# Kernel tuning notes

Hardware: AMD Instinct MI355X
Metric: run time of the kernel (lower is better)

## Reference

```python
import jax, jax.numpy as jnp
import numpy as np

K = 5
PAD = K // 2
EPS = 1e-12  # F.normalize eps


def setup_inputs() -> dict:
    key = jax.random.key(0)
    k1, k2, k3 = jax.random.split(key, 3)
    b, c, h, w = 8, 1024, 64, 64
    out_ch = 1024
    feature = jax.random.normal(k1, (b, c, h, w), dtype=jnp.float32)
    # Conv2d(1024 + K*K, out_ch, 1) -> weight [out_ch, 1049], bias [out_ch]
    conv_w = jax.random.normal(k2, (out_ch, c + K * K), dtype=jnp.float32) * 0.02
    conv_b = jax.random.normal(k3, (out_ch,), dtype=jnp.float32) * 0.02
    return {"feature": feature, "conv_w": conv_w, "conv_b": conv_b}


def reference(feature, conv_w, conv_b):
    b, c, h, w = feature.shape
    # L2-normalize over channel dim (F.normalize: x / max(||x||, eps))
    norm = jnp.sqrt(jnp.sum(feature * feature, axis=1, keepdims=True))
    fn = feature / jnp.maximum(norm, EPS)
    fp = jnp.pad(fn, ((0, 0), (0, 0), (PAD, PAD), (PAD, PAD)))
    # 25 shifted correlations; order matches torch loop: index = col*K + row
    corr = jnp.stack(
        [jnp.sum(fp[:, :, r:h + r, cc:w + cc] * fn, axis=1)
         for cc in range(K) for r in range(K)],
        axis=1,
    )  # [b, K*K, h, w]
    cat = jnp.concatenate([feature, corr], axis=1)  # [b, c+K*K, h, w]
    y = jnp.einsum('oc,bchw->bohw', conv_w, cat) + conv_b[None, :, None, None]
    return jax.nn.relu(y)
```

## Files before the change

### kernel.cpp

```cpp
#include <hip/hip_runtime.h>
#include <hip/hip_bf16.h>


typedef __attribute__((ext_vector_type(8))) short short8x;
typedef __attribute__((ext_vector_type(4))) float floatx4;

#define B_   8
#define C_   1024
#define HW_  4096
#define KPAD 1088
#define NT   17

__device__ __forceinline__ unsigned short f2bf(float f) {
  unsigned int u = __float_as_uint(f);
  u += 0x7FFFu + ((u >> 16) & 1u);
  return (unsigned short)(u >> 16);
}

__device__ __forceinline__ void async16(const void* g, void* l) {
  __builtin_amdgcn_global_load_lds(
      (__attribute__((address_space(1))) void*)(void*)g,
      (__attribute__((address_space(3))) void*)l, 16, 0, 0);
}

__device__ __forceinline__ short8x rd16(const char* p) {
  return *(const short8x*)p;
}

__global__ __launch_bounds__(512) void scn_aux(
    const float* __restrict__ f, float* __restrict__ part,
    unsigned short* __restrict__ At) {
  __shared__ float lds2[2][64][65];
  const int n = blockIdx.x;
  const int g = n / 9, r = n - g * 9;
  const int tid = threadIdx.x;

  if (r == 0) {
    const int x = tid & 63;
    const int y = (g & 7) * 8 + (tid >> 6);
    const int cs = (g >> 3) & 7, b = g >> 6;

    const int xs0 = (x + 2 < 64) ? x + 2 : 63;
    const int xs1 = (x + 1 < 64) ? x + 1 : 63;
    const int xs3 = (x - 1 >= 0) ? x - 1 : 0;
    const int xs4 = (x - 2 >= 0) ? x - 2 : 0;

    const bool ym2 = (y >= 2), ym1 = (y >= 1), yp1 = (y <= 62), yp2 = (y <= 61);

    const float* rp0 = f + ((size_t)b * C_ + cs * 128) * HW_ + y * 64;

    float h[25];
#pragma unroll
    for (int j = 0; j < 25; ++j) h[j] = 0.f;

#pragma unroll 4
    for (int c = 0; c < 128; ++c) {
      const float* rp = rp0 + (size_t)c * HW_;
      const float ctr = rp[x];
      const float vm2 = ym2 ? rp[x - 128] : 0.f;
      const float vm1 = ym1 ? rp[x - 64] : 0.f;
      const float vp1 = yp1 ? rp[x + 64] : 0.f;
      const float vp2 = yp2 ? rp[x + 128] : 0.f;
      const float c0 = __shfl(ctr, xs0, 64);
      const float c1 = __shfl(ctr, xs1, 64);
      const float c3 = __shfl(ctr, xs3, 64);
      const float c4 = __shfl(ctr, xs4, 64);
      const float v[5] = {vm2, vm1, ctr, vp1, vp2};
      const float cc[5] = {c0, c1, ctr, c3, c4};
#pragma unroll
      for (int dxi = 0; dxi < 5; ++dxi)
#pragma unroll
        for (int dyi = 0; dyi < 5; ++dyi)
          h[dxi * 5 + dyi] = fmaf(v[dyi], cc[dxi], h[dxi * 5 + dyi]);
    }

    float* pb = part + (size_t)(cs * 25) * 32768 + b * HW_ + y * 64;
#pragma unroll
    for (int j = 0; j < 25; ++j) {
      const int dx = (j / 5) - 2;
      const int tgt = x - dx;
      const int wx = (tgt + 64) & 63;
      const float val = ((unsigned)tgt < 64u) ? h[j] : 0.f;
      pb[(size_t)j * 32768 + wx] = val;
    }
  } else {
    const int half = tid >> 8, t256 = tid & 255;
    const int tile = (g * 8 + (r - 1)) * 2 + half;
    const int b = tile >> 10, rem = tile & 1023;
    const int kt = rem >> 6, mt = rem & 63;

    const float* src = f + ((size_t)b * C_ + kt * 64) * HW_ + mt * 64;
    const int mi = t256 & 63, kr = t256 >> 6;
#pragma unroll
    for (int i = 0; i < 16; ++i)
      lds2[half][kr + i * 4][mi] = src[(size_t)(kr + i * 4) * HW_ + mi];
    __syncthreads();
    unsigned short* dst = At + ((size_t)b * HW_ + mt * 64) * KPAD + kt * 64;
    const int c = t256 & 7, mr = t256 >> 3;
#pragma unroll
    for (int h2 = 0; h2 < 2; ++h2) {
      const int mm = mr + h2 * 32;
      short8x v;
#pragma unroll
      for (int j = 0; j < 8; ++j) v[j] = (short)f2bf(lds2[half][c * 8 + j][mm]);
      *(short8x*)(dst + (size_t)mm * KPAD + c * 8) = v;
    }
  }
}

__global__ __launch_bounds__(256) void scn_invn(const float* __restrict__ part,
                                                float* __restrict__ invn) {
  const int i = blockIdx.x * 256 + threadIdx.x;
  float s = 0.f;
#pragma unroll
  for (int cs = 0; cs < 8; ++cs) s += part[(size_t)(cs * 25 + 12) * 32768 + i];
  invn[i] = 1.0f / fmaxf(sqrtf(s), 1e-12f);
}

__global__ __launch_bounds__(256) void scn_corr_reduce(
    const float* __restrict__ part, const float* __restrict__ invn,
    unsigned short* __restrict__ At) {
  const int b = blockIdx.y;
  const int m = blockIdx.x * 256 + threadIdx.x;
  const int i = b * HW_ + m;
  const int y = m >> 6, x = m & 63;

  float acc[25];
#pragma unroll
  for (int j = 0; j < 25; ++j) acc[j] = 0.f;
#pragma unroll 1
  for (int cs = 0; cs < 8; ++cs) {
    const float* pb = part + (size_t)(cs * 25) * 32768 + i;
#pragma unroll
    for (int j = 0; j < 25; ++j) acc[j] += pb[(size_t)j * 32768];
  }
  const float ic = invn[i];
  unsigned short r[64];
#pragma unroll
  for (int j = 0; j < 25; ++j) {
    const int dy = (j % 5) - 2, dx = (j / 5) - 2;
    const int ny = y + dy, nx = x + dx;
    float in2 = (ny >= 0 && ny < 64 && nx >= 0 && nx < 64)
                    ? invn[b * HW_ + (ny << 6) + nx] : 0.f;
    r[j] = f2bf(acc[j] * ic * in2);
  }
#pragma unroll
  for (int j = 25; j < 64; ++j) r[j] = 0;
  unsigned short* row = At + ((size_t)b * HW_ + m) * KPAD + 1024;
#pragma unroll
  for (int v = 0; v < 8; ++v) *(short8x*)(row + v * 8) = *(short8x*)(r + v * 8);
}

__global__ __launch_bounds__(256) void scn_wcast(const float* __restrict__ w,
                                                 unsigned short* __restrict__ Wb) {
  const int i = blockIdx.x * 256 + threadIdx.x;
  const int o = i / KPAD, k = i - o * KPAD;
  Wb[i] = (k < 1049) ? f2bf(w[(size_t)o * 1049 + k]) : 0;
}

__global__ __launch_bounds__(512, 2) void scn_gemm(
    const unsigned short* __restrict__ Wb, const unsigned short* __restrict__ At,
    const float* __restrict__ bias, float* __restrict__ out) {
  extern __shared__ char lds[];
  const int tid = threadIdx.x;
  const int l = tid & 63;
  const int wid = tid >> 6;
  const int wm = wid >> 2;
  const int wn = wid & 3;
  const int nb = blockIdx.x, ob = blockIdx.y, b = blockIdx.z;

  const int rr = tid >> 3;
  const int cswz = ((tid & 7) ^ (rr & 7)) << 3;
  const unsigned short* gA = Wb + (size_t)(ob * 256 + rr) * KPAD + cswz;
  const unsigned short* gB = At + ((size_t)b * HW_ + nb * 256 + rr) * KPAD + cswz;
  char* const dBase = (char*)lds + tid * 16;

#define ISSUE_A(bf, kt)                                         \
  do {                                                          \
    const unsigned short* _s = gA + (kt) * 64;                  \
    char* _d = dBase + (bf) * 65536;                            \
    async16(_s, _d);                                            \
    async16(_s + (size_t)64 * KPAD, _d + 8192);                 \
    async16(_s + (size_t)128 * KPAD, _d + 16384);               \
    async16(_s + (size_t)192 * KPAD, _d + 24576);               \
  } while (0)

#define ISSUE_B(bf, kt)                                         \
  do {                                                          \
    const unsigned short* _s = gB + (kt) * 64;                  \
    char* _d = dBase + (bf) * 65536 + 32768;                    \
    async16(_s, _d);                                            \
    async16(_s + (size_t)64 * KPAD, _d + 8192);                 \
    async16(_s + (size_t)128 * KPAD, _d + 16384);               \
    async16(_s + (size_t)192 * KPAD, _d + 24576);               \
  } while (0)

  const int l15 = l & 15, l4g = l >> 4, l7 = l & 7;
  const int aoff0 = l15 * 128 + ((l4g ^ l7) << 4);
  const int aoff1 = l15 * 128 + (((l4g + 4) ^ l7) << 4);
  const char* aB0 = (const char*)lds + wm * 16384;
  const char* bB0 = (const char*)lds + 32768 + (wn >> 1) * 16384 + (wn & 1) * 8192;

  floatx4 acc[8][4];
#pragma unroll
  for (int i = 0; i < 8; ++i)
#pragma unroll
    for (int j = 0; j < 4; ++j) acc[i][j] = (floatx4){0.f, 0.f, 0.f, 0.f};

  ISSUE_A(0, 0); ISSUE_B(0, 0);
  ISSUE_A(1, 1); ISSUE_B(1, 1);
  asm volatile("s_waitcnt vmcnt(8)" ::: "memory");
  __builtin_amdgcn_s_barrier();

  short8x a[4][2], b0[2][2], b1[2][2];

  for (int t = 0; t < NT; ++t) {
    const int bf = t & 1;
    const char* ab = aB0 + bf * 65536;
    const char* bb = bB0 + bf * 65536;
    const int t2 = (t < NT - 2) ? (t + 2) : 0;

#pragma unroll
    for (int i = 0; i < 4; ++i) {
      a[i][0] = rd16(ab + i * 2048 + aoff0);
      a[i][1] = rd16(ab + i * 2048 + aoff1);
    }
#pragma unroll
    for (int j = 0; j < 2; ++j) {
      b0[j][0] = rd16(bb + j * 2048 + aoff0);
      b0[j][1] = rd16(bb + j * 2048 + aoff1);
    }
    __builtin_amdgcn_s_barrier();
    asm volatile("s_waitcnt lgkmcnt(0)" ::: "memory");
    __builtin_amdgcn_sched_barrier(0);
    __builtin_amdgcn_s_setprio(1);
#pragma unroll
    for (int i = 0; i < 4; ++i)
#pragma unroll
      for (int j = 0; j < 2; ++j) {
        acc[i][j] = __builtin_amdgcn_mfma_f32_16x16x32_bf16(a[i][0], b0[j][0], acc[i][j], 0, 0, 0);
        acc[i][j] = __builtin_amdgcn_mfma_f32_16x16x32_bf16(a[i][1], b0[j][1], acc[i][j], 0, 0, 0);
      }
    __builtin_amdgcn_s_setprio(0);
    __builtin_amdgcn_s_barrier();

#pragma unroll
    for (int j = 0; j < 2; ++j) {
      b1[j][0] = rd16(bb + (2 + j) * 2048 + aoff0);
      b1[j][1] = rd16(bb + (2 + j) * 2048 + aoff1);
    }
    __builtin_amdgcn_s_barrier();
    asm volatile("s_waitcnt lgkmcnt(0)" ::: "memory");
    __builtin_amdgcn_sched_barrier(0);
    __builtin_amdgcn_s_setprio(1);
#pragma unroll
    for (int i = 0; i < 4; ++i)
#pragma unroll
      for (int j = 0; j < 2; ++j) {
        acc[i][2 + j] = __builtin_amdgcn_mfma_f32_16x16x32_bf16(a[i][0], b1[j][0], acc[i][2 + j], 0, 0, 0);
        acc[i][2 + j] = __builtin_amdgcn_mfma_f32_16x16x32_bf16(a[i][1], b1[j][1], acc[i][2 + j], 0, 0, 0);
      }
    __builtin_amdgcn_s_setprio(0);
    __builtin_amdgcn_s_barrier();

#pragma unroll
    for (int i = 0; i < 4; ++i) {
      a[i][0] = rd16(ab + (4 + i) * 2048 + aoff0);
      a[i][1] = rd16(ab + (4 + i) * 2048 + aoff1);
    }
    ISSUE_B(bf, t2);
    __builtin_amdgcn_s_barrier();
    asm volatile("s_waitcnt lgkmcnt(0)" ::: "memory");
    __builtin_amdgcn_sched_barrier(0);
    __builtin_amdgcn_s_setprio(1);
#pragma unroll
    for (int i = 0; i < 4; ++i)
#pragma unroll
      for (int j = 0; j < 2; ++j) {
        acc[4 + i][2 + j] = __builtin_amdgcn_mfma_f32_16x16x32_bf16(a[i][0], b1[j][0], acc[4 + i][2 + j], 0, 0, 0);
        acc[4 + i][2 + j] = __builtin_amdgcn_mfma_f32_16x16x32_bf16(a[i][1], b1[j][1], acc[4 + i][2 + j], 0, 0, 0);
      }
    __builtin_amdgcn_s_setprio(0);
    __builtin_amdgcn_s_barrier();

    ISSUE_A(bf, t2);
    __builtin_amdgcn_s_barrier();
    __builtin_amdgcn_s_setprio(1);
#pragma unroll
    for (int i = 0; i < 4; ++i)
#pragma unroll
      for (int j = 0; j < 2; ++j) {
        acc[4 + i][j] = __builtin_amdgcn_mfma_f32_16x16x32_bf16(a[i][0], b0[j][0], acc[4 + i][j], 0, 0, 0);
        acc[4 + i][j] = __builtin_amdgcn_mfma_f32_16x16x32_bf16(a[i][1], b0[j][1], acc[4 + i][j], 0, 0, 0);
      }
    __builtin_amdgcn_s_setprio(0);
    asm volatile("s_waitcnt vmcnt(8)" ::: "memory");
    __builtin_amdgcn_s_barrier();
  }
  asm volatile("s_waitcnt vmcnt(0)" ::: "memory");
#undef ISSUE_A
#undef ISSUE_B

  float* outb = out + (size_t)b * C_ * HW_;
#pragma unroll
  for (int i = 0; i < 8; ++i) {
    const int o0 = ob * 256 + wm * 128 + i * 16 + l4g * 4;
    float bs[4];
#pragma unroll
    for (int r = 0; r < 4; ++r) bs[r] = bias[o0 + r];
#pragma unroll
    for (int j = 0; j < 4; ++j) {
      const int m = nb * 256 + wn * 64 + j * 16 + l15;
#pragma unroll
      for (int r = 0; r < 4; ++r) {
        float v = acc[i][j][r] + bs[r];
        outb[(size_t)(o0 + r) * HW_ + m] = v > 0.f ? v : 0.f;
      }
    }
  }
}

extern "C" void kernel_launch(void* const* d_in, const int* in_sizes, int n_in,
                              void* d_out, int out_size, void* d_ws, size_t ws_size,
                              hipStream_t stream) {
  const float* feature = (const float*)d_in[0];
  const float* conv_w  = (const float*)d_in[1];
  const float* conv_b  = (const float*)d_in[2];
  float* out = (float*)d_out;

  char* ws = (char*)d_ws;
  unsigned short* At = (unsigned short*)(ws);
  float* part        = (float*)(ws + 71303168);
  unsigned short* Wb = (unsigned short*)(ws + 71303168);
  float* invn        = (float*)(ws + 97517568);

  static int gemm_attr_set = 0;
  if (!gemm_attr_set) {
    hipFuncSetAttribute((const void*)scn_gemm,
                        hipFuncAttributeMaxDynamicSharedMemorySize, 131072);
    gemm_attr_set = 1;
  }

  scn_aux<<<dim3(4608), 512, 0, stream>>>(feature, part, At);
  scn_invn<<<dim3(128), 256, 0, stream>>>(part, invn);
  scn_corr_reduce<<<dim3(16, 8), 256, 0, stream>>>(part, invn, At);
  scn_wcast<<<dim3((1024 * KPAD) / 256), 256, 0, stream>>>(conv_w, Wb);
  scn_gemm<<<dim3(16, 4, 8), 512, 131072, stream>>>(Wb, At, conv_b, out);
}
```

Baseline: 388.3 us.

## Fuse weight cast into aux kernel, atomically accumulate correlations, merge reduce kernels

Correlation partials from the eight channel slices are now summed with atomicAdd into one zeroed buffer instead of written as separate slices, so the separate inverse-norm pass is no longer needed. The inverse-norm and correlation-reduce kernels become one kernel that computes inverse norms for a row halo in LDS. The weight cast to bf16 moves into extra blocks of the aux kernel with 8-wide stores, and the transpose loads become float4. Together these cut kernel launches and traffic on the partial buffer, at the cost of a memset, atomic contention, and ordering nondeterminism in the float sums.

New measurement: 379.0 us. -2.4%, faster.

```diff
diff --git a/kernel.cpp b/kernel.cpp
--- a/kernel.cpp
+++ b/kernel.cpp
@@ -28,13 +28,27 @@
 }
 
 __global__ __launch_bounds__(512) void scn_aux(
-    const float* __restrict__ f, float* __restrict__ part,
-    unsigned short* __restrict__ At) {
+    const float* __restrict__ f, float* __restrict__ corr,
+    unsigned short* __restrict__ At, const float* __restrict__ w,
+    unsigned short* __restrict__ Wb) {
   __shared__ float lds2[2][64][65];
   const int n = blockIdx.x;
+  const int tid = threadIdx.x;
+
+  if (n >= 4608) {
+    const int base = (n - 4608) * 4096 + tid * 8;
+    const int o = base / KPAD, kk = base - o * KPAD;
+    short8x v;
+#pragma unroll
+    for (int e = 0; e < 8; ++e) {
+      const int k = kk + e;
+      v[e] = (k < 1049) ? (short)f2bf(w[(size_t)o * 1049 + k]) : (short)0;
+    }
+    *(short8x*)(Wb + (size_t)o * KPAD + kk) = v;
+    return;
+  }
+
   const int g = n / 9, r = n - g * 9;
-  const int tid = threadIdx.x;
-
   if (r == 0) {
     const int x = tid & 63;
     const int y = (g & 7) * 8 + (tid >> 6);
@@ -74,14 +88,14 @@
           h[dxi * 5 + dyi] = fmaf(v[dyi], cc[dxi], h[dxi * 5 + dyi]);
     }
 
-    float* pb = part + (size_t)(cs * 25) * 32768 + b * HW_ + y * 64;
+    float* pb = corr + b * HW_ + y * 64;
 #pragma unroll
     for (int j = 0; j < 25; ++j) {
       const int dx = (j / 5) - 2;
       const int tgt = x - dx;
       const int wx = (tgt + 64) & 63;
       const float val = ((unsigned)tgt < 64u) ? h[j] : 0.f;
-      pb[(size_t)j * 32768 + wx] = val;
+      atomicAdd(pb + (size_t)j * 32768 + wx, val);
     }
   } else {
     const int half = tid >> 8, t256 = tid & 255;
@@ -89,11 +103,14 @@
     const int b = tile >> 10, rem = tile & 1023;
     const int kt = rem >> 6, mt = rem & 63;
 
-    const float* src = f + ((size_t)b * C_ + kt * 64) * HW_ + mt * 64;
-    const int mi = t256 & 63, kr = t256 >> 6;
-#pragma unroll
-    for (int i = 0; i < 16; ++i)
-      lds2[half][kr + i * 4][mi] = src[(size_t)(kr + i * 4) * HW_ + mi];
+    const int m4 = (t256 & 15) << 2, kr0 = t256 >> 4;
+    const float* src = f + ((size_t)b * C_ + kt * 64 + kr0) * HW_ + mt * 64 + m4;
+#pragma unroll
+    for (int i = 0; i < 4; ++i) {
+      floatx4 v = *(const floatx4*)(src + (size_t)i * 16 * HW_);
+      float* d = &lds2[half][kr0 + i * 16][m4];
+      d[0] = v[0]; d[1] = v[1]; d[2] = v[2]; d[3] = v[3];
+    }
     __syncthreads();
     unsigned short* dst = At + ((size_t)b * HW_ + mt * 64) * KPAD + kt * 64;
     const int c = t256 & 7, mr = t256 >> 3;
@@ -108,54 +125,45 @@
   }
 }
 
-__global__ __launch_bounds__(256) void scn_invn(const float* __restrict__ part,
-                                                float* __restrict__ invn) {
-  const int i = blockIdx.x * 256 + threadIdx.x;
-  float s = 0.f;
-#pragma unroll
-  for (int cs = 0; cs < 8; ++cs) s += part[(size_t)(cs * 25 + 12) * 32768 + i];
-  invn[i] = 1.0f / fmaxf(sqrtf(s), 1e-12f);
-}
-
-__global__ __launch_bounds__(256) void scn_corr_reduce(
-    const float* __restrict__ part, const float* __restrict__ invn,
-    unsigned short* __restrict__ At) {
+__global__ __launch_bounds__(256) void scn_reduce2(
+    const float* __restrict__ corr, unsigned short* __restrict__ At) {
+  __shared__ float linv[8][64];
   const int b = blockIdx.y;
-  const int m = blockIdx.x * 256 + threadIdx.x;
+  const int bx = blockIdx.x;
+  const int tid = threadIdx.x;
+  const int x = tid & 63;
+  const int y0 = bx * 4;
+
+  const float* c12 = corr + (size_t)12 * 32768 + b * HW_;
+#pragma unroll
+  for (int rr = 0; rr < 2; ++rr) {
+    const int rsel = (tid >> 6) + rr * 4;
+    const int yy = y0 - 2 + rsel;
+    const float s = (yy >= 0 && yy < 64) ? c12[yy * 64 + x] : 1.0f;
+    linv[rsel][x] = 1.0f / fmaxf(sqrtf(s), 1e-12f);
+  }
+  __syncthreads();
+
+  const int m = bx * 256 + tid;
   const int i = b * HW_ + m;
-  const int y = m >> 6, x = m & 63;
-
-  float acc[25];
-#pragma unroll
-  for (int j = 0; j < 25; ++j) acc[j] = 0.f;
-#pragma unroll 1
-  for (int cs = 0; cs < 8; ++cs) {
-    const float* pb = part + (size_t)(cs * 25) * 32768 + i;
-#pragma unroll
-    for (int j = 0; j < 25; ++j) acc[j] += pb[(size_t)j * 32768];
-  }
-  const float ic = invn[i];
+  const int yr = tid >> 6;
+  const float ic = linv[yr + 2][x];
+
   unsigned short r[64];
 #pragma unroll
   for (int j = 0; j < 25; ++j) {
+    const float acc = corr[(size_t)j * 32768 + i];
     const int dy = (j % 5) - 2, dx = (j / 5) - 2;
-    const int ny = y + dy, nx = x + dx;
-    float in2 = (ny >= 0 && ny < 64 && nx >= 0 && nx < 64)
-                    ? invn[b * HW_ + (ny << 6) + nx] : 0.f;
-    r[j] = f2bf(acc[j] * ic * in2);
+    const int ny = y0 + yr + dy, nx = x + dx;
+    const float in2 = (ny >= 0 && ny < 64 && nx >= 0 && nx < 64)
+                          ? linv[yr + 2 + dy][nx] : 0.f;
+    r[j] = f2bf(acc * ic * in2);
   }
 #pragma unroll
   for (int j = 25; j < 64; ++j) r[j] = 0;
   unsigned short* row = At + ((size_t)b * HW_ + m) * KPAD + 1024;
 #pragma unroll
   for (int v = 0; v < 8; ++v) *(short8x*)(row + v * 8) = *(short8x*)(r + v * 8);
-}
-
-__global__ __launch_bounds__(256) void scn_wcast(const float* __restrict__ w,
-                                                 unsigned short* __restrict__ Wb) {
-  const int i = blockIdx.x * 256 + threadIdx.x;
-  const int o = i / KPAD, k = i - o * KPAD;
-  Wb[i] = (k < 1049) ? f2bf(w[(size_t)o * 1049 + k]) : 0;
 }
 
 __global__ __launch_bounds__(512, 2) void scn_gemm(
@@ -330,9 +338,8 @@
 
   char* ws = (char*)d_ws;
   unsigned short* At = (unsigned short*)(ws);
-  float* part        = (float*)(ws + 71303168);
-  unsigned short* Wb = (unsigned short*)(ws + 71303168);
-  float* invn        = (float*)(ws + 97517568);
+  float* corr        = (float*)(ws + 71303168);
+  unsigned short* Wb = (unsigned short*)(ws + 74579968);
 
   static int gemm_attr_set = 0;
   if (!gemm_attr_set) {
@@ -341,9 +348,8 @@
     gemm_attr_set = 1;
   }
 
-  scn_aux<<<dim3(4608), 512, 0, stream>>>(feature, part, At);
-  scn_invn<<<dim3(128), 256, 0, stream>>>(part, invn);
-  scn_corr_reduce<<<dim3(16, 8), 256, 0, stream>>>(part, invn, At);
-  scn_wcast<<<dim3((1024 * KPAD) / 256), 256, 0, stream>>>(conv_w, Wb);
+  hipMemsetAsync(corr, 0, 25 * 32768 * sizeof(float), stream);
+  scn_aux<<<dim3(4880), 512, 0, stream>>>(feature, corr, At, conv_w, Wb);
+  scn_reduce2<<<dim3(16, 8), 256, 0, stream>>>(corr, At);
   scn_gemm<<<dim3(16, 4, 8), 512, 131072, stream>>>(Wb, At, conv_b, out);
 }
```
